# Optimization experiments

Measured on AMD Instinct MI355X. Metric: run time of the kernel, lower is better.

## Reference

```python
import jax, jax.numpy as jnp
import numpy as np

R = 64
HIDDEN = 4096
N_HEADS = 32
SEQ = 16384


def setup_inputs() -> dict:
    key = jax.random.key(0)
    ks = jax.random.split(key, 8)
    d = HIDDEN
    inv = 1.0 / np.sqrt(d)
    return {
        "query": jax.random.normal(ks[0], (SEQ, d), dtype=jnp.float32),
        "kv_latent": jax.random.normal(ks[1], (R, d), dtype=jnp.float32),
        "wq": jax.random.normal(ks[2], (d, d), dtype=jnp.float32) * inv,
        "wo": jax.random.normal(ks[3], (d, d), dtype=jnp.float32) * inv,
        "w1": jax.random.normal(ks[4], (d, d), dtype=jnp.float32) * inv,
        "b1": jnp.zeros((d,), dtype=jnp.float32),
        "w2": jax.random.normal(ks[5], (d, d), dtype=jnp.float32) * inv,
        "b2": jnp.zeros((d,), dtype=jnp.float32),
    }


def reference(query, kv_latent, wq, wo, w1, b1, w2, b2):
    S, d = query.shape
    H = N_HEADS
    dh = d // H
    scale = R ** (-0.5)  # note: original scales by r**-0.5, not head_dim
    # query projection -> per-head queries [S, H, dh]
    xq = (query @ wq).reshape(S, H, dh) * scale
    kv = kv_latent.reshape(R, H, dh)  # shared key = value latents
    # attention over the r latents, per head
    attn = jnp.einsum("shd,rhd->shr", xq, kv)
    attn = jax.nn.softmax(attn, axis=-1)
    out = jnp.einsum("shr,rhd->shd", attn, kv).reshape(S, d)
    out = out @ wo
    # residual MLP block with exact (erf) GELU
    h = jax.nn.gelu(out @ w1 + b1, approximate=False)
    return (h @ w2 + b2) + out
```

## Files before the change

kernel.cpp:

```cpp
#include <hip/hip_runtime.h>
#include <hip/hip_bf16.h>
#include <math.h>

#define SEQ   16384
#define DDIM  4096
#define NH    32
#define DH    128
#define RLAT  64

using u16 = unsigned short;
typedef __attribute__((ext_vector_type(8))) short short8;
typedef __attribute__((ext_vector_type(4))) float f32x4;

__device__ __forceinline__ u16 f2bf(float x) {
  __hip_bfloat16 b = __float2bfloat16(x);
  return *reinterpret_cast<u16*>(&b);
}
__device__ __forceinline__ float bf2f(u16 u) {
  __hip_bfloat16 b;
  *reinterpret_cast<u16*>(&b) = u;
  return __bfloat162float(b);
}

#define GLD16(gp, lp)                                                        \
  __builtin_amdgcn_global_load_lds(                                          \
      (const __attribute__((address_space(1))) unsigned int*)(gp),           \
      (__attribute__((address_space(3))) unsigned int*)(lp), 16, 0, 0)

template <int EPI>
__global__ __launch_bounds__(512, 2) void gemm_split(
    const u16* __restrict__ Ah, const u16* __restrict__ Al,
    const u16* __restrict__ Bh, const u16* __restrict__ Bl,
    float* __restrict__ Cf, u16* __restrict__ Ch, u16* __restrict__ Cl,
    const float* __restrict__ bias, const u16* __restrict__ Rh,
    const u16* __restrict__ Rl, float scale) {
  __shared__ __align__(16) u16 smem[2][4][8192];

  const int tid = threadIdx.x;
  const int lane = tid & 63;
  const int w = tid >> 6;
  const int wm = w >> 2, wn = w & 3;

  const int bid = blockIdx.x;
  const int wg = (bid & 7) * 128 + (bid >> 3);
  const int bm = (wg >> 4) * 256;
  const int bn = (wg & 15) * 256;

  const int kblk = (lane & 3) ^ ((lane >> 3) & 3);
  const int grow = w * 16 + (lane >> 2);
  const u16* gAh = Ah + (size_t)(bm + grow) * DDIM + kblk * 8;
  const u16* gAl = Al + (size_t)(bm + grow) * DDIM + kblk * 8;
  const u16* gBh = Bh + (size_t)(bn + grow) * DDIM + kblk * 8;
  const u16* gBl = Bl + (size_t)(bn + grow) * DDIM + kblk * 8;
  const int ldso = w * 16 * 32;

  const int r15 = lane & 15, kb = lane >> 4;
  const int sphys = (kb ^ ((r15 >> 1) & 3)) * 8;

  f32x4 acc[8][4] = {};

#pragma unroll
  for (int c = 0; c < 2; ++c) {
    const size_t go = (size_t)c * 128 * DDIM;
    const int lo = ldso + c * 128 * 32;
    GLD16(gAh + go, &smem[0][0][lo]);
    GLD16(gAl + go, &smem[0][1][lo]);
    GLD16(gBh + go, &smem[0][2][lo]);
    GLD16(gBl + go, &smem[0][3][lo]);
  }
  asm volatile("s_waitcnt vmcnt(0)" ::: "memory");
  __builtin_amdgcn_s_barrier();

  for (int t = 0; t < 128; ++t) {
    const u16* br = &smem[t & 1][0][0];
    u16* bw = &smem[(t + 1) & 1][0][0];
    const int k0n = (t + 1) * 32;
#pragma unroll
    for (int p = 0; p < 4; ++p) {
      if (p == 0 && t < 127) {
#pragma unroll
        for (int c = 0; c < 2; ++c) {
          const size_t go = (size_t)c * 128 * DDIM + k0n;
          const int lo = ldso + c * 128 * 32;
          GLD16(gAh + go, bw + 0 * 8192 + lo);
          GLD16(gAl + go, bw + 1 * 8192 + lo);
          GLD16(gBh + go, bw + 2 * 8192 + lo);
          GLD16(gBl + go, bw + 3 * 8192 + lo);
        }
      }
      short8 xah[4], xal[4], xbh[2], xbl[2];
#pragma unroll
      for (int mi = 0; mi < 4; ++mi) {
        const int row = wm * 128 + (p & 1) * 64 + mi * 16 + r15;
        xah[mi] = *(const short8*)(br + 0 * 8192 + row * 32 + sphys);
        xal[mi] = *(const short8*)(br + 1 * 8192 + row * 32 + sphys);
      }
#pragma unroll
      for (int ni = 0; ni < 2; ++ni) {
        const int row = wn * 64 + (p >> 1) * 32 + ni * 16 + r15;
        xbh[ni] = *(const short8*)(br + 2 * 8192 + row * 32 + sphys);
        xbl[ni] = *(const short8*)(br + 3 * 8192 + row * 32 + sphys);
      }
      __builtin_amdgcn_s_barrier();
      __builtin_amdgcn_s_setprio(1);
#pragma unroll
      for (int mi = 0; mi < 4; ++mi)
#pragma unroll
        for (int ni = 0; ni < 2; ++ni) {
          f32x4& a = acc[(p & 1) * 4 + mi][(p >> 1) * 2 + ni];
          a = __builtin_amdgcn_mfma_f32_16x16x32_bf16(xah[mi], xbh[ni], a, 0, 0, 0);
          a = __builtin_amdgcn_mfma_f32_16x16x32_bf16(xah[mi], xbl[ni], a, 0, 0, 0);
          a = __builtin_amdgcn_mfma_f32_16x16x32_bf16(xal[mi], xbh[ni], a, 0, 0, 0);
        }
      __builtin_amdgcn_s_setprio(0);
      __builtin_amdgcn_s_barrier();
    }
    asm volatile("s_waitcnt vmcnt(0)" ::: "memory");
    __builtin_amdgcn_s_barrier();
  }

  const int orow = bm + wm * 128 + kb * 4;
  const int ocol = bn + wn * 64 + r15;
#pragma unroll
  for (int mi = 0; mi < 8; ++mi)
#pragma unroll
    for (int ni = 0; ni < 4; ++ni)
#pragma unroll
      for (int q = 0; q < 4; ++q) {
        const size_t row = (size_t)(orow + mi * 16 + q);
        const size_t col = (size_t)(ocol + ni * 16);
        const size_t o = row * DDIM + col;
        float v = acc[mi][ni][q];
        if (EPI == 0) {
          Cf[o] = v * scale;
        } else if (EPI == 1) {
          u16 h = f2bf(v);
          Ch[o] = h;
          Cl[o] = f2bf(v - bf2f(h));
        } else if (EPI == 2) {
          v += bias[col];
          v = 0.5f * v * (1.0f + erff(v * 0.70710678118654752f));
          u16 h = f2bf(v);
          Ch[o] = h;
          Cl[o] = f2bf(v - bf2f(h));
        } else {
          v += bias[col] + bf2f(Rh[o]) + bf2f(Rl[o]);
          Cf[o] = v;
        }
      }
}

__global__ __launch_bounds__(256) void attn_k(const float* __restrict__ xq,
                                              const float* __restrict__ kvl,
                                              u16* __restrict__ oh,
                                              u16* __restrict__ ol) {
  __shared__ float kv_s[RLAT * 129];
  __shared__ float xrow[4][DH];
  __shared__ float pbuf[4][RLAT];

  const int h = blockIdx.y;
  const int s0 = blockIdx.x * 64;
  const int tid = threadIdx.x;

#pragma unroll
  for (int i = 0; i < 32; ++i) {
    int idx = i * 256 + tid;
    int r = idx >> 7, d = idx & 127;
    kv_s[r * 129 + d] = kvl[(size_t)r * DDIM + h * DH + d];
  }
  __syncthreads();

  const int wave = tid >> 6;
  const int lane = tid & 63;

  for (int it = 0; it < 16; ++it) {
    const int s = s0 + wave * 16 + it;
    const size_t base = (size_t)s * DDIM + h * DH;
    xrow[wave][lane] = xq[base + lane];
    xrow[wave][lane + 64] = xq[base + lane + 64];

    float sc = 0.f;
    const float* kr = &kv_s[lane * 129];
#pragma unroll 8
    for (int d = 0; d < DH; ++d) sc = fmaf(xrow[wave][d], kr[d], sc);

    float mx = sc;
#pragma unroll
    for (int off = 32; off; off >>= 1) mx = fmaxf(mx, __shfl_xor(mx, off));
    float p = expf(sc - mx);
    float sm = p;
#pragma unroll
    for (int off = 32; off; off >>= 1) sm += __shfl_xor(sm, off);
    p /= sm;
    pbuf[wave][lane] = p;

    float a0 = 0.f, a1 = 0.f;
#pragma unroll 8
    for (int r = 0; r < RLAT; ++r) {
      float pv = pbuf[wave][r];
      a0 = fmaf(pv, kv_s[r * 129 + lane], a0);
      a1 = fmaf(pv, kv_s[r * 129 + lane + 64], a1);
    }
    u16 h0 = f2bf(a0);
    oh[base + lane] = h0;
    ol[base + lane] = f2bf(a0 - bf2f(h0));
    u16 h1 = f2bf(a1);
    oh[base + lane + 64] = h1;
    ol[base + lane + 64] = f2bf(a1 - bf2f(h1));
  }
}

__global__ __launch_bounds__(256) void conv_split(const float* __restrict__ in,
                                                  u16* __restrict__ oh,
                                                  u16* __restrict__ ol,
                                                  long n4) {
  long i = (long)blockIdx.x * blockDim.x + threadIdx.x;
  const long stride = (long)gridDim.x * blockDim.x;
  for (; i < n4; i += stride) {
    float4 v = ((const float4*)in)[i];
    u16 h0 = f2bf(v.x), h1 = f2bf(v.y), h2 = f2bf(v.z), h3 = f2bf(v.w);
    u16 l0 = f2bf(v.x - bf2f(h0)), l1 = f2bf(v.y - bf2f(h1));
    u16 l2 = f2bf(v.z - bf2f(h2)), l3 = f2bf(v.w - bf2f(h3));
    uint2 hp, lp;
    hp.x = (uint)h0 | ((uint)h1 << 16);
    hp.y = (uint)h2 | ((uint)h3 << 16);
    lp.x = (uint)l0 | ((uint)l1 << 16);
    lp.y = (uint)l2 | ((uint)l3 << 16);
    ((uint2*)oh)[i] = hp;
    ((uint2*)ol)[i] = lp;
  }
}

__global__ __launch_bounds__(256) void conv_wT(const float* __restrict__ w,
                                               u16* __restrict__ oh,
                                               u16* __restrict__ ol) {
  __shared__ float t[64][65];
  const int kb = blockIdx.x & 63, nb = blockIdx.x >> 6;
  const int tid = threadIdx.x;
#pragma unroll
  for (int j = 0; j < 16; ++j) {
    int idx = j * 256 + tid;
    int r = idx >> 6, c = idx & 63;
    t[r][c] = w[(size_t)(kb * 64 + r) * DDIM + nb * 64 + c];
  }
  __syncthreads();
#pragma unroll
  for (int j = 0; j < 16; ++j) {
    int idx = j * 256 + tid;
    int r = idx >> 6, c = idx & 63;
    float v = t[c][r];
    u16 h = f2bf(v);
    size_t o = (size_t)(nb * 64 + r) * DDIM + kb * 64 + c;
    oh[o] = h;
    ol[o] = f2bf(v - bf2f(h));
  }
}

extern "C" void kernel_launch(void* const* d_in, const int* in_sizes, int n_in,
                              void* d_out, int out_size, void* d_ws, size_t ws_size,
                              hipStream_t stream) {
  const float* query = (const float*)d_in[0];
  const float* kvl   = (const float*)d_in[1];
  const float* wq    = (const float*)d_in[2];
  const float* wo    = (const float*)d_in[3];
  const float* w1    = (const float*)d_in[4];
  const float* b1    = (const float*)d_in[5];
  const float* w2    = (const float*)d_in[6];
  const float* b2    = (const float*)d_in[7];
  float* out = (float*)d_out;

  char* ws = (char*)d_ws;
  const size_t HB = (size_t)SEQ * DDIM * sizeof(u16);
  const size_t WB = (size_t)DDIM * DDIM * sizeof(u16);

  u16* qh  = (u16*)(ws);
  u16* ql  = (u16*)(ws + HB);
  u16* ath = qh;  u16* atl = ql;
  u16* hh  = qh;  u16* hl  = ql;
  float* xqf = (float*)(ws + 2 * HB);
  u16* o2h = (u16*)(ws + 2 * HB);
  u16* o2l = (u16*)(ws + 3 * HB);
  char* wr = ws + 4 * HB;
  u16* wqh = (u16*)(wr + 0 * WB); u16* wql = (u16*)(wr + 1 * WB);
  u16* woh = (u16*)(wr + 2 * WB); u16* wol = (u16*)(wr + 3 * WB);
  u16* w1h = (u16*)(wr + 4 * WB); u16* w1l = (u16*)(wr + 5 * WB);
  u16* w2h = (u16*)(wr + 6 * WB); u16* w2l = (u16*)(wr + 7 * WB);

  const long n4 = (long)SEQ * DDIM / 4;
  conv_split<<<8192, 256, 0, stream>>>(query, qh, ql, n4);
  conv_wT<<<4096, 256, 0, stream>>>(wq, wqh, wql);
  conv_wT<<<4096, 256, 0, stream>>>(wo, woh, wol);
  conv_wT<<<4096, 256, 0, stream>>>(w1, w1h, w1l);
  conv_wT<<<4096, 256, 0, stream>>>(w2, w2h, w2l);

  const dim3 gg(1024), gb(512);
  gemm_split<0><<<gg, gb, 0, stream>>>(qh, ql, wqh, wql, xqf, nullptr, nullptr,
                                       nullptr, nullptr, nullptr, 0.125f);
  attn_k<<<dim3(SEQ / 64, NH), 256, 0, stream>>>(xqf, kvl, ath, atl);
  gemm_split<1><<<gg, gb, 0, stream>>>(ath, atl, woh, wol, nullptr, o2h, o2l,
                                       nullptr, nullptr, nullptr, 1.f);
  gemm_split<2><<<gg, gb, 0, stream>>>(o2h, o2l, w1h, w1l, nullptr, hh, hl,
                                       b1, nullptr, nullptr, 1.f);
  gemm_split<3><<<gg, gb, 0, stream>>>(hh, hl, w2h, w2l, out, nullptr, nullptr,
                                       b2, o2h, o2l, 1.f);
}
```

Before: 7.721 ms.

## Split split-bf16 GEMM k-step into hi/lo phases with staged async loads

```diff
diff --git a/kernel.cpp b/kernel.cpp
--- a/kernel.cpp
+++ b/kernel.cpp
@@ -64,60 +64,89 @@
     const size_t go = (size_t)c * 128 * DDIM;
     const int lo = ldso + c * 128 * 32;
     GLD16(gAh + go, &smem[0][0][lo]);
+    GLD16(gBh + go, &smem[0][2][lo]);
+  }
+#pragma unroll
+  for (int c = 0; c < 2; ++c) {
+    const size_t go = (size_t)c * 128 * DDIM;
+    const int lo = ldso + c * 128 * 32;
     GLD16(gAl + go, &smem[0][1][lo]);
-    GLD16(gBh + go, &smem[0][2][lo]);
     GLD16(gBl + go, &smem[0][3][lo]);
   }
-  asm volatile("s_waitcnt vmcnt(0)" ::: "memory");
   __builtin_amdgcn_s_barrier();
 
   for (int t = 0; t < 128; ++t) {
     const u16* br = &smem[t & 1][0][0];
     u16* bw = &smem[(t + 1) & 1][0][0];
-    const int k0n = (t + 1) * 32;
-#pragma unroll
-    for (int p = 0; p < 4; ++p) {
-      if (p == 0 && t < 127) {
-#pragma unroll
-        for (int c = 0; c < 2; ++c) {
-          const size_t go = (size_t)c * 128 * DDIM + k0n;
-          const int lo = ldso + c * 128 * 32;
-          GLD16(gAh + go, bw + 0 * 8192 + lo);
-          GLD16(gAl + go, bw + 1 * 8192 + lo);
-          GLD16(gBh + go, bw + 2 * 8192 + lo);
-          GLD16(gBl + go, bw + 3 * 8192 + lo);
+    const int k0n = (t < 127 ? t + 1 : 127) * 32;
+
+#pragma unroll
+    for (int c = 0; c < 2; ++c) {
+      const size_t go = (size_t)c * 128 * DDIM + k0n;
+      const int lo = ldso + c * 128 * 32;
+      GLD16(gAh + go, bw + 0 * 8192 + lo);
+      GLD16(gBh + go, bw + 2 * 8192 + lo);
+    }
+    asm volatile("s_waitcnt vmcnt(8)" ::: "memory");
+    __builtin_amdgcn_s_barrier();
+
+    short8 fBh[4];
+#pragma unroll
+    for (int ni = 0; ni < 4; ++ni)
+      fBh[ni] = *(const short8*)(br + 2 * 8192 + (wn * 64 + ni * 16 + r15) * 32 + sphys);
+    __builtin_amdgcn_s_setprio(1);
+#pragma unroll
+    for (int mh = 0; mh < 2; ++mh) {
+      short8 fAh[4];
+#pragma unroll
+      for (int mi = 0; mi < 4; ++mi)
+        fAh[mi] = *(const short8*)(br + 0 * 8192 + (wm * 128 + mh * 64 + mi * 16 + r15) * 32 + sphys);
+#pragma unroll
+      for (int ni = 0; ni < 4; ++ni)
+#pragma unroll
+        for (int mi = 0; mi < 4; ++mi)
+          acc[mh * 4 + mi][ni] =
+              __builtin_amdgcn_mfma_f32_16x16x32_bf16(fAh[mi], fBh[ni], acc[mh * 4 + mi][ni], 0, 0, 0);
+    }
+    __builtin_amdgcn_s_setprio(0);
+
+#pragma unroll
+    for (int c = 0; c < 2; ++c) {
+      const size_t go = (size_t)c * 128 * DDIM + k0n;
+      const int lo = ldso + c * 128 * 32;
+      GLD16(gAl + go, bw + 1 * 8192 + lo);
+      GLD16(gBl + go, bw + 3 * 8192 + lo);
+    }
+    asm volatile("s_waitcnt vmcnt(8)" ::: "memory");
+    __builtin_amdgcn_s_barrier();
+
+    short8 fBl[4];
+#pragma unroll
+    for (int ni = 0; ni < 4; ++ni)
+      fBl[ni] = *(const short8*)(br + 3 * 8192 + (wn * 64 + ni * 16 + r15) * 32 + sphys);
+    __builtin_amdgcn_s_setprio(1);
+#pragma unroll
+    for (int mh = 0; mh < 2; ++mh) {
+      short8 fAh[4], fAl[4];
+#pragma unroll
+      for (int mi = 0; mi < 4; ++mi) {
+        const int row = wm * 128 + mh * 64 + mi * 16 + r15;
+        fAh[mi] = *(const short8*)(br + 0 * 8192 + row * 32 + sphys);
+        fAl[mi] = *(const short8*)(br + 1 * 8192 + row * 32 + sphys);
+      }
+#pragma unroll
+      for (int ni = 0; ni < 4; ++ni)
+#pragma unroll
+        for (int mi = 0; mi < 4; ++mi) {
+          f32x4& a = acc[mh * 4 + mi][ni];
+          a = __builtin_amdgcn_mfma_f32_16x16x32_bf16(fAh[mi], fBl[ni], a, 0, 0, 0);
+          a = __builtin_amdgcn_mfma_f32_16x16x32_bf16(fAl[mi], fBh[ni], a, 0, 0, 0);
         }
-      }
-      short8 xah[4], xal[4], xbh[2], xbl[2];
-#pragma unroll
-      for (int mi = 0; mi < 4; ++mi) {
-        const int row = wm * 128 + (p & 1) * 64 + mi * 16 + r15;
-        xah[mi] = *(const short8*)(br + 0 * 8192 + row * 32 + sphys);
-        xal[mi] = *(const short8*)(br + 1 * 8192 + row * 32 + sphys);
-      }
-#pragma unroll
-      for (int ni = 0; ni < 2; ++ni) {
-        const int row = wn * 64 + (p >> 1) * 32 + ni * 16 + r15;
-        xbh[ni] = *(const short8*)(br + 2 * 8192 + row * 32 + sphys);
-        xbl[ni] = *(const short8*)(br + 3 * 8192 + row * 32 + sphys);
-      }
-      __builtin_amdgcn_s_barrier();
-      __builtin_amdgcn_s_setprio(1);
-#pragma unroll
-      for (int mi = 0; mi < 4; ++mi)
-#pragma unroll
-        for (int ni = 0; ni < 2; ++ni) {
-          f32x4& a = acc[(p & 1) * 4 + mi][(p >> 1) * 2 + ni];
-          a = __builtin_amdgcn_mfma_f32_16x16x32_bf16(xah[mi], xbh[ni], a, 0, 0, 0);
-          a = __builtin_amdgcn_mfma_f32_16x16x32_bf16(xah[mi], xbl[ni], a, 0, 0, 0);
-          a = __builtin_amdgcn_mfma_f32_16x16x32_bf16(xal[mi], xbh[ni], a, 0, 0, 0);
-        }
-      __builtin_amdgcn_s_setprio(0);
-      __builtin_amdgcn_s_barrier();
-    }
-    asm volatile("s_waitcnt vmcnt(0)" ::: "memory");
+    }
+    __builtin_amdgcn_s_setprio(0);
     __builtin_amdgcn_s_barrier();
   }
+  asm volatile("s_waitcnt vmcnt(0)" ::: "memory");
 
   const int orow = bm + wm * 128 + kb * 4;
   const int ocol = bn + wn * 64 + r15;
```

Measured after the change: 6.857 ms. 1.13x faster.
